# Performance work log

Hardware: AMD Instinct MI355X
Metric: run time of the kernel (lower is better)

The kernel has to match this reference:

```python
import jax, jax.numpy as jnp
import numpy as np

ALPHABET = 26

def _shift(position, S):
    if position == 0:
        return jnp.zeros(S, dtype=jnp.int32)
    elif position == 1:
        return jnp.arange(S, dtype=jnp.int32) % ALPHABET
    elif position == 2:
        return jnp.arange(S, dtype=jnp.int32) // 26 + 1 % 26  # faithful to torch precedence: +1
    elif position == 3:
        return jnp.arange(S, dtype=jnp.int32) // 676 + 1 % 26
    raise ValueError('Invalid rotor position')


def setup_inputs() -> dict:
    key = jax.random.key(0)
    k1, k2 = jax.random.split(key)
    B, S = 128, 8192
    signalInput = jax.random.normal(k1, (B, S, ALPHABET), dtype=jnp.float32)
    # xavier_normal_ on a 26x26 matrix: std = sqrt(2/(26+26))
    std = float(np.sqrt(2.0 / (ALPHABET + ALPHABET)))
    rotor = jax.random.normal(k2, (ALPHABET, ALPHABET), dtype=jnp.float32) * std
    return {"signalInput": signalInput, "rotor": rotor}


def reference(signalInput, rotor):
    position = 1
    B, S, _ = signalInput.shape
    # L2-normalize rotor rows (torch.norm(dim=1, keepdim=True))
    rn = rotor / jnp.linalg.norm(rotor, axis=1, keepdims=True)  # [26,26]
    shift = _shift(position, S)                                  # [S]
    # one_hot((i + shift[s]) % 26) @ rn  ==  gather rn rows
    idx = (jnp.arange(ALPHABET, dtype=jnp.int32)[None, :] + shift[:, None]) % ALPHABET  # [S,26]
    M = rn[idx]                                                  # [S,26,26]
    # per-token 1x26 @ 26x26 bmm, batch-independent rotation matrix
    out = jnp.einsum('bsi,sij->bsj', signalInput, M)             # [B,S,26]
    return jax.nn.softmax(out, axis=2)
```

## Files before the change

### kernel.cpp

```cpp
#include <hip/hip_runtime.h>
#include <math.h>

#define ALPHA 26
#define ROW_PAD 32
#define TPB 256
#define TOK_PAD 27

__global__ void rotor_norm_kernel(const float* __restrict__ rotor,
                                  float* __restrict__ rn) {
    int i = threadIdx.x;
    if (i < ALPHA) {
        float ss = 0.f;
        #pragma unroll
        for (int j = 0; j < ALPHA; ++j) {
            float v = rotor[i * ALPHA + j];
            ss += v * v;
        }
        float inv = 1.0f / sqrtf(ss);
        #pragma unroll
        for (int j = 0; j < ALPHA; ++j)
            rn[i * ROW_PAD + j] = rotor[i * ALPHA + j] * inv;
    }
}

__global__ __launch_bounds__(TPB) void rotor_main(
        const float* __restrict__ x,
        const float* __restrict__ rn,
        float* __restrict__ out) {
    __shared__ float tile[TPB * TOK_PAD];

    const int tid = threadIdx.x;
    const long long blockTok = (long long)blockIdx.x * TPB;
    const float* gin = x + blockTok * ALPHA;
    float* gout = out + blockTok * ALPHA;

    #pragma unroll
    for (int it = 0; it < 13; ++it) {
        int v = tid + it * TPB;
        int f = v * 2;
        int tok = f / ALPHA;
        int el = f - tok * ALPHA;
        float2 d = *(const float2*)(gin + f);
        float* p = &tile[tok * TOK_PAD + el];
        p[0] = d.x;
        p[1] = d.y;
    }
    __syncthreads();

    const int n = (int)blockTok + tid;
    const int s = n & 8191;
    const int r = s % 26;

    float acc[ALPHA];
    #pragma unroll
    for (int j = 0; j < ALPHA; ++j) acc[j] = 0.f;

    const float* myx = &tile[tid * TOK_PAD];
    int idx = 26 - r; if (idx == 26) idx = 0;
    for (int k = 0; k < ALPHA; ++k) {
        float xk = myx[idx];
        ++idx; if (idx == ALPHA) idx = 0;
        const float* row = rn + k * ROW_PAD;
        #pragma unroll
        for (int j = 0; j < ALPHA; ++j)
            acc[j] = fmaf(xk, row[j], acc[j]);
    }

    float m = acc[0];
    #pragma unroll
    for (int j = 1; j < ALPHA; ++j) m = fmaxf(m, acc[j]);
    float sum = 0.f;
    #pragma unroll
    for (int j = 0; j < ALPHA; ++j) { acc[j] = __expf(acc[j] - m); sum += acc[j]; }
    float inv = 1.0f / sum;
    #pragma unroll
    for (int j = 0; j < ALPHA; ++j) acc[j] *= inv;

    __syncthreads();
    #pragma unroll
    for (int j = 0; j < ALPHA; ++j)
        tile[tid * TOK_PAD + j] = acc[j];
    __syncthreads();

    #pragma unroll
    for (int it = 0; it < 13; ++it) {
        int v = tid + it * TPB;
        int f = v * 2;
        int tok = f / ALPHA;
        int el = f - tok * ALPHA;
        float2 d;
        d.x = tile[tok * TOK_PAD + el];
        d.y = tile[tok * TOK_PAD + el + 1];
        *(float2*)(gout + f) = d;
    }
}

extern "C" void kernel_launch(void* const* d_in, const int* in_sizes, int n_in,
                              void* d_out, int out_size, void* d_ws, size_t ws_size,
                              hipStream_t stream) {
    const float* x     = (const float*)d_in[0];
    const float* rotor = (const float*)d_in[1];
    float* out = (float*)d_out;
    float* rn  = (float*)d_ws;

    rotor_norm_kernel<<<1, 64, 0, stream>>>(rotor, rn);

    const int tokens = out_size / ALPHA;
    const int blocks = tokens / TPB;
    rotor_main<<<blocks, TPB, 0, stream>>>(x, rn, out);
}
```

Before: 203.2 us.

## Load input tile via global_load_lds and use float4 unpadded LDS staging

```diff
diff --git a/kernel.cpp b/kernel.cpp
--- a/kernel.cpp
+++ b/kernel.cpp
@@ -4,7 +4,10 @@
 #define ALPHA 26
 #define ROW_PAD 32
 #define TPB 256
-#define TOK_PAD 27
+#define TILE_FLOATS (TPB * ALPHA)
+
+typedef __attribute__((address_space(3))) float lds_f;
+typedef const __attribute__((address_space(1))) float glb_f;
 
 __global__ void rotor_norm_kernel(const float* __restrict__ rotor,
                                   float* __restrict__ rn) {
@@ -27,43 +30,54 @@
         const float* __restrict__ x,
         const float* __restrict__ rn,
         float* __restrict__ out) {
-    __shared__ float tile[TPB * TOK_PAD];
+    __shared__ float tile[TILE_FLOATS];
 
     const int tid = threadIdx.x;
+    const int wave = tid >> 6;
     const long long blockTok = (long long)blockIdx.x * TPB;
     const float* gin = x + blockTok * ALPHA;
     float* gout = out + blockTok * ALPHA;
 
     #pragma unroll
-    for (int it = 0; it < 13; ++it) {
-        int v = tid + it * TPB;
-        int f = v * 2;
-        int tok = f / ALPHA;
-        int el = f - tok * ALPHA;
-        float2 d = *(const float2*)(gin + f);
-        float* p = &tile[tok * TOK_PAD + el];
-        p[0] = d.x;
-        p[1] = d.y;
+    for (int it = 0; it < 6; ++it) {
+        int v4 = it * TPB + tid;
+        __builtin_amdgcn_global_load_lds(
+            (glb_f*)(gin + v4 * 4),
+            (lds_f*)&tile[(it * TPB + wave * 64) * 4],
+            16, 0, 0);
+    }
+    if (tid < 128) {
+        int v4 = 6 * TPB + tid;
+        __builtin_amdgcn_global_load_lds(
+            (glb_f*)(gin + v4 * 4),
+            (lds_f*)&tile[(6 * TPB + wave * 64) * 4],
+            16, 0, 0);
     }
     __syncthreads();
 
     const int n = (int)blockTok + tid;
-    const int s = n & 8191;
-    const int r = s % 26;
+    const int r = (n & 8191) % 26;
+    int shift = 26 - r; if (shift == 26) shift = 0;
+
+    const float* myx = &tile[tid * ALPHA];
+    float xv[ALPHA];
+    #pragma unroll
+    for (int k = 0; k < ALPHA; ++k) {
+        int idx = k + shift;
+        idx = (idx >= ALPHA) ? idx - ALPHA : idx;
+        xv[k] = myx[idx];
+    }
 
     float acc[ALPHA];
     #pragma unroll
     for (int j = 0; j < ALPHA; ++j) acc[j] = 0.f;
 
-    const float* myx = &tile[tid * TOK_PAD];
-    int idx = 26 - r; if (idx == 26) idx = 0;
+    #pragma unroll
     for (int k = 0; k < ALPHA; ++k) {
-        float xk = myx[idx];
-        ++idx; if (idx == ALPHA) idx = 0;
-        const float* row = rn + k * ROW_PAD;
+        const float xk = xv[k];
         #pragma unroll
         for (int j = 0; j < ALPHA; ++j)
-            acc[j] = fmaf(xk, row[j], acc[j]);
+            acc[j] = fmaf(xk, rn[k * ROW_PAD + j], acc[j]);
     }
 
     float m = acc[0];
@@ -79,19 +93,19 @@
     __syncthreads();
     #pragma unroll
     for (int j = 0; j < ALPHA; ++j)
-        tile[tid * TOK_PAD + j] = acc[j];
+        tile[tid * ALPHA + j] = acc[j];
     __syncthreads();
 
     #pragma unroll
-    for (int it = 0; it < 13; ++it) {
-        int v = tid + it * TPB;
-        int f = v * 2;
-        int tok = f / ALPHA;
-        int el = f - tok * ALPHA;
-        float2 d;
-        d.x = tile[tok * TOK_PAD + el];
-        d.y = tile[tok * TOK_PAD + el + 1];
-        *(float2*)(gout + f) = d;
+    for (int it = 0; it < 6; ++it) {
+        int v4 = it * TPB + tid;
+        float4 d = *(const float4*)&tile[v4 * 4];
+        *(float4*)(gout + v4 * 4) = d;
+    }
+    if (tid < 128) {
+        int v4 = 6 * TPB + tid;
+        float4 d = *(const float4*)&tile[v4 * 4];
+        *(float4*)(gout + v4 * 4) = d;
     }
 }
 
```

Measured after the change: 204.5 us. About the same (+0.6%).
